# Kernel optimization log

Measured on AMD Instinct MI355X. Metric: run time of the kernel, lower is better.

The kernel has to match this reference:

```python
import jax, jax.numpy as jnp
import numpy as np
from jax import lax

D = 33            # n_vertices
NEG_SLOPE = 0.2   # LeakyReLU slope
EPS_IN = 1e-5     # InstanceNorm eps


def _block(x, w, b, gamma, beta):
    # Conv2d(k=3, stride=2, pad=1) -> LeakyReLU(0.2) -> optional InstanceNorm2d(affine)
    y = lax.conv_general_dilated(x, w, (2, 2), [(1, 1), (1, 1)],
                                 dimension_numbers=('NCHW', 'OIHW', 'NCHW'))
    y = y + b[None, :, None, None]
    y = jnp.where(y >= 0, y, NEG_SLOPE * y)
    if gamma is not None:
        mu = jnp.mean(y, (2, 3), keepdims=True)
        var = jnp.var(y, (2, 3), keepdims=True)
        y = (y - mu) * lax.rsqrt(var + EPS_IN) * gamma[None, :, None, None] + beta[None, :, None, None]
    return y


def _backbone(lq, w1, b1, g1, be1, w2, b2, g2, be2, w3, b3, g3, be3,
              w4, b4, g4, be4, w5, b5):
    B = lq.shape[0]
    # F.interpolate(..., 256, bilinear, align_corners=False) == half-pixel linear, no antialias
    x = jax.image.resize(lq, (B, 3, 256, 256), method='linear', antialias=False)
    x = _block(x, w1, b1, g1, be1)   # [B,16,128,128]
    x = _block(x, w2, b2, g2, be2)   # [B,32,64,64]
    x = _block(x, w3, b3, g3, be3)   # [B,64,32,32]
    x = _block(x, w4, b4, g4, be4)   # [B,128,16,16]
    x = _block(x, w5, b5, None, None)  # [B,128,8,8]; Dropout is identity in eval
    # AdaptiveAvgPool2d(2) on 8x8 -> mean over 4x4 blocks
    x = x.reshape(B, 128, 2, 4, 2, 4).mean((3, 5))  # [B,128,2,2]
    return x.reshape(B, -1)  # [B,512]


def _trilerp(lut, r, g, b):
    # lut [3,D,D,D]; r,g,b [N] in [0, D-1]; align_corners=True + border padding
    i0 = jnp.clip(jnp.floor(r).astype(jnp.int32), 0, D - 2)
    j0 = jnp.clip(jnp.floor(g).astype(jnp.int32), 0, D - 2)
    k0 = jnp.clip(jnp.floor(b).astype(jnp.int32), 0, D - 2)
    fr, fg, fb = r - i0, g - j0, b - k0

    def c(di, dj, dk):
        return lut[:, i0 + di, j0 + dj, k0 + dk]  # [3,N]

    return (c(0, 0, 0) * (1 - fr) * (1 - fg) * (1 - fb)
            + c(0, 0, 1) * (1 - fr) * (1 - fg) * fb
            + c(0, 1, 0) * (1 - fr) * fg * (1 - fb)
            + c(0, 1, 1) * (1 - fr) * fg * fb
            + c(1, 0, 0) * fr * (1 - fg) * (1 - fb)
            + c(1, 0, 1) * fr * (1 - fg) * fb
            + c(1, 1, 0) * fr * fg * (1 - fb)
            + c(1, 1, 1) * fr * fg * fb)


def _ailut_transform(img, luts, vertices):
    # img [B,3,H,W] in [0,1]; luts [B,3,D,D,D]; vertices [B,3,D] sorted in [0,1]
    B, C, H, W = img.shape
    p = img.reshape(B, C, -1)  # [B,3,N]
    # per-(b,c) searchsorted(right=True)
    idx = jax.vmap(jax.vmap(lambda v, x: jnp.searchsorted(v, x, side='right')))(vertices, p)
    idx = jnp.clip(idx, 1, D - 1)
    v_lo = jnp.take_along_axis(vertices, idx - 1, axis=-1)
    v_hi = jnp.take_along_axis(vertices, idx, axis=-1)
    frac = (p - v_lo) / (v_hi - v_lo + 1e-8)
    coord = (idx - 1).astype(img.dtype) + frac        # [B,3,N] in [0, D-1]
    coord = jnp.clip(coord, 0.0, D - 1.0)             # border padding
    # torch grid layout (blue->W, green->H, red->D); LUT axes are (red, green, blue)
    sampled = jax.vmap(_trilerp)(luts, coord[:, 0], coord[:, 1], coord[:, 2])  # [B,3,N]
    return sampled.reshape(B, C, H, W)


def _forward(lq, w1, b1, g1, be1, w2, b2, g2, be2, w3, b3, g3, be3,
             w4, b4, g4, be4, w5, b5, lw, lb, bw, aw, ab):
    B = lq.shape[0]
    codes = _backbone(lq, w1, b1, g1, be1, w2, b2, g2, be2, w3, b3, g3, be3,
                      w4, b4, g4, be4, w5, b5)          # [B,512]
    # LUTGenerator
    weights = codes @ lw.T + lb                          # [B,3]
    luts = (weights @ bw.T).reshape(B, 3, D, D, D)       # [B,3,D,D,D]
    # AdaInt
    intervals = (codes @ aw.T + ab).reshape(B, 3, D - 1)
    intervals = jax.nn.softmax(intervals, axis=-1)
    vertices = jnp.pad(jnp.cumsum(intervals, axis=-1), ((0, 0), (0, 0), (1, 0)))  # [B,3,D]
    outs = jnp.clip(_ailut_transform(lq, luts, vertices), 0.0, 1.0)
    return outs, weights, vertices


def setup_inputs() -> dict:
    key = jax.random.key(0)
    ks = jax.random.split(key, 16)
    B = 4
    lq = jax.random.uniform(ks[0], (B, 3, 1024, 1024), jnp.float32)

    def cw(k, o, i):
        return jax.random.normal(k, (o, i, 3, 3), jnp.float32) * (1.0 / np.sqrt(i * 9))

    w1 = cw(ks[1], 16, 3);   b1 = jnp.zeros(16);  g1 = jnp.ones(16);  be1 = jnp.zeros(16)
    w2 = cw(ks[2], 32, 16);  b2 = jnp.zeros(32);  g2 = jnp.ones(32);  be2 = jnp.zeros(32)
    w3 = cw(ks[3], 64, 32);  b3 = jnp.zeros(64);  g3 = jnp.ones(64);  be3 = jnp.zeros(64)
    w4 = cw(ks[4], 128, 64); b4 = jnp.zeros(128); g4 = jnp.ones(128); be4 = jnp.zeros(128)
    w5 = cw(ks[5], 128, 128); b5 = jnp.zeros(128)

    lw = jax.random.normal(ks[6], (3, 512), jnp.float32) * 0.02
    lb = jnp.ones(3, jnp.float32)  # init: bias = ones
    # basis LUT bank: rank0 = identity LUT (meshgrid/(D-1), channel-flipped), others small
    grid = jnp.stack(jnp.meshgrid(jnp.arange(D), jnp.arange(D), jnp.arange(D),
                                  indexing='ij'), 0).astype(jnp.float32) / (D - 1)
    identity = grid[::-1].reshape(-1, 1)  # [3*D^3,1]
    bw = jnp.concatenate([identity,
                          jax.random.normal(ks[7], (3 * D ** 3, 2), jnp.float32) * 0.01], axis=1)
    aw = jax.random.normal(ks[8], (96, 512), jnp.float32) * 0.01
    ab = jnp.ones(96, jnp.float32)  # init: bias = ones
    return {'lq': lq, 'w1': w1, 'b1': b1, 'g1': g1, 'be1': be1,
            'w2': w2, 'b2': b2, 'g2': g2, 'be2': be2,
            'w3': w3, 'b3': b3, 'g3': g3, 'be3': be3,
            'w4': w4, 'b4': b4, 'g4': g4, 'be4': be4,
            'w5': w5, 'b5': b5, 'lw': lw, 'lb': lb, 'bw': bw, 'aw': aw, 'ab': ab}


def reference(lq, w1, b1, g1, be1, w2, b2, g2, be2, w3, b3, g3, be3,
              w4, b4, g4, be4, w5, b5, lw, lb, bw, aw, ab):
    return _forward(lq, w1, b1, g1, be1, w2, b2, g2, be2, w3, b3, g3, be3,
                    w4, b4, g4, be4, w5, b5, lw, lb, bw, aw, ab)
```

## Files before the change

### kernel.cpp

```cpp
#include <hip/hip_runtime.h>
#include <math.h>

#define LUT_D 33
#define LUT_D3 35937
#define NEG 0.2f
#define BATCH 4
#define HW_IMG 1048576

__global__ void k_resize(const float* __restrict__ lq, float* __restrict__ out) {
    int gid = blockIdx.x * 256 + threadIdx.x;
    if (gid >= BATCH * 3 * 256 * 256) return;
    int x  = gid & 255;
    int y  = (gid >> 8) & 255;
    int pc = gid >> 16;
    const float* in = lq + (size_t)pc * HW_IMG;
    const float* p0 = in + (4 * y + 1) * 1024 + (4 * x + 1);
    out[gid] = 0.25f * (p0[0] + p0[1] + p0[1024] + p0[1025]);
}

template<int IC, int OC, int OH, int OW, int NSPLIT, bool NORM_IN, bool STATS_OUT>
__global__ void __launch_bounds__(256) k_conv_t(
    const float* __restrict__ in, const float* __restrict__ nrm_in,
    const float* __restrict__ w, const float* __restrict__ bias,
    float* __restrict__ out, float* __restrict__ part) {
    constexpr int IH = OH * 2, IW = OW * 2;
    constexpr int ICB = IC / NSPLIT;
    constexpr int TROW = 20, TSZ = 17 * TROW;
    constexpr int WQ = ICB * 9 / 4;
    constexpr int NTX = OW / 8, NTY = OH / 8, NOCG = OC / 16;
    constexpr int NT = NTX * NTY;
    constexpr int PX = OH * OW;

    __shared__ float sIn[ICB * TSZ];
    __shared__ float swl[16 * ICB * 9];
    __shared__ float sNm[NORM_IN ? ICB * 2 : 1];

    int id = blockIdx.x;
    int ocg   = id % NOCG;   id /= NOCG;
    int icc_i = id % NSPLIT; id /= NSPLIT;
    int tx    = id % NTX;    id /= NTX;
    int ty    = id % NTY;    id /= NTY;
    int b     = id;
    int icc   = icc_i * ICB;

    int t    = threadIdx.x;
    int lane = t >> 6;
    int px   = t & 63;
    int py   = px >> 3, pxx = px & 7;
    int oc0  = ocg * 16 + lane * 4;

    if (IC == ICB) {
        const float4* wsrc = (const float4*)(w + (size_t)ocg * 16 * IC * 9);
        for (int i = t; i < 16 * IC * 9 / 4; i += 256) ((float4*)swl)[i] = wsrc[i];
    } else {
        for (int i = t; i < 16 * WQ; i += 256) {
            int ol = i / WQ, qi = i % WQ;
            ((float4*)swl)[ol * WQ + qi] =
                *(const float4*)(w + ((size_t)(ocg * 16 + ol) * IC + icc) * 9 + qi * 4);
        }
    }
    if (NORM_IN) {
        for (int i = t; i < ICB * 2; i += 256) sNm[i] = nrm_in[(b * IC + icc) * 2 + i];
    }
    __syncthreads();

    int iy0 = ty * 16 - 1;
    int xbase = tx * 16;
    const float* inb = in + (size_t)(b * IC + icc) * (IH * IW);
    for (int q = t; q < ICB * 17 * 4; q += 256) {
        int ic_l = q / 68;
        int r    = q % 68;
        int row  = r >> 2, quad = r & 3;
        int iy = iy0 + row;
        float4 v = {0.f, 0.f, 0.f, 0.f};
        if (iy >= 0 && iy < IH) {
            v = *(const float4*)(inb + (size_t)ic_l * (IH * IW) + (size_t)iy * IW + xbase + quad * 4);
            if (NORM_IN) {
                float sc = sNm[ic_l * 2], sh = sNm[ic_l * 2 + 1];
                v.x = v.x * sc + sh; v.y = v.y * sc + sh;
                v.z = v.z * sc + sh; v.w = v.w * sc + sh;
            }
        }
        *(float4*)(sIn + ic_l * TSZ + row * TROW + 4 + quad * 4) = v;
    }
    for (int h = t; h < ICB * 17; h += 256) {
        int ic_l = h / 17, row = h % 17;
        int iy = iy0 + row, ix = xbase - 1;
        float v = 0.f;
        if (iy >= 0 && iy < IH && ix >= 0) {
            v = inb[(size_t)ic_l * (IH * IW) + (size_t)iy * IW + ix];
            if (NORM_IN) v = v * sNm[ic_l * 2] + sNm[ic_l * 2 + 1];
        }
        sIn[ic_l * TSZ + row * TROW + 3] = v;
    }
    __syncthreads();

    float acc[4];
    #pragma unroll
    for (int j = 0; j < 4; j++) acc[j] = (NSPLIT == 1) ? bias[oc0 + j] : 0.f;

    for (int i2 = 0; i2 < ICB; i2++) {
        const float* tp = sIn + i2 * TSZ + py * 2 * TROW + pxx * 2 + 3;
        float x0 = tp[0],        x1 = tp[1],        x2 = tp[2];
        float x3 = tp[TROW],     x4 = tp[TROW + 1], x5 = tp[TROW + 2];
        float x6 = tp[2 * TROW], x7 = tp[2 * TROW + 1], x8 = tp[2 * TROW + 2];
        #pragma unroll
        for (int j = 0; j < 4; j++) {
            const float* wp = swl + ((lane * 4 + j) * ICB + i2) * 9;
            acc[j] = fmaf(x0, wp[0], acc[j]);
            acc[j] = fmaf(x1, wp[1], acc[j]);
            acc[j] = fmaf(x2, wp[2], acc[j]);
            acc[j] = fmaf(x3, wp[3], acc[j]);
            acc[j] = fmaf(x4, wp[4], acc[j]);
            acc[j] = fmaf(x5, wp[5], acc[j]);
            acc[j] = fmaf(x6, wp[6], acc[j]);
            acc[j] = fmaf(x7, wp[7], acc[j]);
            acc[j] = fmaf(x8, wp[8], acc[j]);
        }
    }

    int oy = ty * 8 + py, ox = tx * 8 + pxx;
    if (NSPLIT == 1) {
        int tile = ty * NTX + tx;
        #pragma unroll
        for (int j = 0; j < 4; j++) {
            float a = acc[j];
            a = a >= 0.f ? a : NEG * a;
            out[((size_t)(b * OC + oc0 + j) * OH + oy) * OW + ox] = a;
            if (STATS_OUT) {
                float s1 = a, s2 = a * a;
                for (int off = 32; off > 0; off >>= 1) {
                    s1 += __shfl_down(s1, off, 64);
                    s2 += __shfl_down(s2, off, 64);
                }
                if (px == 0) {
                    size_t pi = ((size_t)(b * OC + oc0 + j) * NT + tile) * 2;
                    part[pi] = s1; part[pi + 1] = s2;
                }
            }
        }
    } else {
        #pragma unroll
        for (int j = 0; j < 4; j++) {
            part[(size_t)icc_i * (BATCH * OC * PX) +
                 (size_t)(b * OC + oc0 + j) * PX + oy * OW + ox] = acc[j];
        }
    }
}

template<int NSPLIT, int OC, int PX, bool STATS>
__global__ void k_combine(const float* __restrict__ ps, const float* __restrict__ bias,
                          float* __restrict__ out, float* __restrict__ spart) {
    constexpr int TOT = BATCH * OC * PX;
    int e = blockIdx.x * 256 + threadIdx.x;
    if (e >= TOT) return;
    float s = 0.f;
    #pragma unroll
    for (int k = 0; k < NSPLIT; k++) s += ps[(size_t)k * TOT + e];
    int oc = (e / PX) % OC;
    s += bias[oc];
    s = s >= 0.f ? s : NEG * s;
    out[e] = s;
    if (STATS) {
        float s1 = s, s2 = s * s;
        for (int off = 32; off > 0; off >>= 1) {
            s1 += __shfl_down(s1, off, 64);
            s2 += __shfl_down(s2, off, 64);
        }
        if ((threadIdx.x & 63) == 0) {
            int widx = e >> 6;
            spart[widx * 2] = s1; spart[widx * 2 + 1] = s2;
        }
    }
}

template<int NT>
__global__ void k_norm(const float* __restrict__ part, const float* __restrict__ g,
                       const float* __restrict__ be, float invN, int C,
                       float* __restrict__ nrm) {
    int bc = blockIdx.x;
    int t  = threadIdx.x;
    float s1 = 0.f, s2 = 0.f;
    for (int i = t; i < NT; i += 64) {
        s1 += part[((size_t)bc * NT + i) * 2];
        s2 += part[((size_t)bc * NT + i) * 2 + 1];
    }
    #pragma unroll
    for (int off = 32; off > 0; off >>= 1) {
        s1 += __shfl_down(s1, off, 64);
        s2 += __shfl_down(s2, off, 64);
    }
    if (t == 0) {
        int c = bc % C;
        float m   = s1 * invN;
        float var = s2 * invN - m * m;
        float sc  = g[c] * rsqrtf(var + 1e-5f);
        nrm[bc * 2]     = sc;
        nrm[bc * 2 + 1] = be[c] - m * sc;
    }
}

__global__ void k_pool(const float* __restrict__ f5, float* __restrict__ codes) {
    int c = blockIdx.x * 256 + threadIdx.x;
    if (c >= 2048) return;
    int b = c >> 9;
    int rest = c & 511;
    int oc = rest >> 2, q = rest & 3;
    int py = (q >> 1) * 4, px = (q & 1) * 4;
    const float* p = f5 + ((size_t)(b * 128 + oc)) * 64;
    float s = 0.f;
    #pragma unroll
    for (int dy = 0; dy < 4; dy++)
        #pragma unroll
        for (int dx = 0; dx < 4; dx++)
            s += p[(py + dy) * 8 + px + dx];
    codes[c] = s * (1.f / 16.f);
}

__global__ void k_head(const float* __restrict__ codes, const float* __restrict__ lw,
                       const float* __restrict__ lb, const float* __restrict__ aw,
                       const float* __restrict__ ab, float* __restrict__ wt,
                       float* __restrict__ vert, float* __restrict__ out_w,
                       float* __restrict__ out_v) {
    int blk = blockIdx.x;
    int t = threadIdx.x;
    if (blk == 12) {
        if (t < 12) {
            int b = t / 3, j = t % 3;
            const float* c = codes + b * 512;
            const float* l = lw + j * 512;
            float s = lb[j];
            for (int k = 0; k < 512; k++) s += c[k] * l[k];
            wt[t] = s;
            out_w[t] = s;
        }
        return;
    }
    int b = blk / 3, ch = blk % 3;
    __shared__ float y[32];
    if (t < 32) {
        const float* c = codes + b * 512;
        const float* a = aw + (size_t)(ch * 32 + t) * 512;
        float s = ab[ch * 32 + t];
        for (int k = 0; k < 512; k++) s += c[k] * a[k];
        y[t] = s;
    }
    __syncthreads();
    if (t == 0) {
        float mx = y[0];
        for (int m = 1; m < 32; m++) mx = fmaxf(mx, y[m]);
        float e[32];
        float sum = 0.f;
        for (int m = 0; m < 32; m++) { e[m] = expf(y[m] - mx); sum += e[m]; }
        float inv = 1.f / sum;
        float cum = 0.f;
        float* vb = vert + (b * 3 + ch) * 33;
        float* ob = out_v + (b * 3 + ch) * 33;
        vb[0] = 0.f; ob[0] = 0.f;
        for (int m = 0; m < 32; m++) { cum += e[m] * inv; vb[m + 1] = cum; ob[m + 1] = cum; }
    }
}

__global__ void k_lutgen(const float* __restrict__ bw, const float* __restrict__ wt,
                         float* __restrict__ luts4) {
    int gid = blockIdx.x * 256 + threadIdx.x;
    if (gid >= BATCH * LUT_D3) return;
    int b = gid / LUT_D3;
    int cell = gid - b * LUT_D3;
    float w0 = wt[b * 3], w1 = wt[b * 3 + 1], w2 = wt[b * 3 + 2];
    const float* r0 = bw + (size_t)(0 * LUT_D3 + cell) * 3;
    const float* r1 = bw + (size_t)(1 * LUT_D3 + cell) * 3;
    const float* r2 = bw + (size_t)(2 * LUT_D3 + cell) * 3;
    float4 o;
    o.x = r0[0] * w0 + r0[1] * w1 + r0[2] * w2;
    o.y = r1[0] * w0 + r1[1] * w1 + r1[2] * w2;
    o.z = r2[0] * w0 + r2[1] * w1 + r2[2] * w2;
    o.w = 0.f;
    ((float4*)luts4)[gid] = o;
}

__device__ __forceinline__ void search1(const float* __restrict__ sv, int ch, float x,
                                        int& i0, float& f) {
    const float* v = sv + ch * LUT_D;
    int lo = 0, hi = LUT_D;
    while (lo < hi) { int mid = (lo + hi) >> 1; if (v[mid] <= x) lo = mid + 1; else hi = mid; }
    int idx = lo < 1 ? 1 : (lo > LUT_D - 1 ? LUT_D - 1 : lo);
    float vl = v[idx - 1], vh = v[idx];
    float fr = (x - vl) / (vh - vl + 1e-8f);
    float coord = (float)(idx - 1) + fr;
    coord = fminf(fmaxf(coord, 0.f), (float)(LUT_D - 1));
    i0 = (int)floorf(coord);
    if (i0 > LUT_D - 2) i0 = LUT_D - 2;
    f = coord - (float)i0;
}

__global__ void __launch_bounds__(256) k_transform(const float* __restrict__ lq,
                                                   const float* __restrict__ luts4,
                                                   const float* __restrict__ vert,
                                                   float* __restrict__ out) {
    int bimg = blockIdx.x >> 10;
    int blk  = blockIdx.x & 1023;
    __shared__ float sv[3 * LUT_D];
    if (threadIdx.x < 3 * LUT_D) sv[threadIdx.x] = vert[bimg * 3 * LUT_D + threadIdx.x];
    __syncthreads();
    int p0 = blk * 1024 + threadIdx.x * 4;
    const float* lr = lq + (size_t)bimg * 3 * HW_IMG + p0;
    float4 r4 = *(const float4*)(lr);
    float4 g4 = *(const float4*)(lr + HW_IMG);
    float4 b4 = *(const float4*)(lr + 2 * HW_IMG);
    const float4* L = (const float4*)(luts4 + (size_t)bimg * LUT_D3 * 4);
    float rr[4] = {r4.x, r4.y, r4.z, r4.w};
    float gg[4] = {g4.x, g4.y, g4.z, g4.w};
    float bb[4] = {b4.x, b4.y, b4.z, b4.w};
    float ro[4], go[4], bo[4];
    #pragma unroll
    for (int i = 0; i < 4; i++) {
        int i0, j0, k0; float fr, fg, fb;
        search1(sv, 0, rr[i], i0, fr);
        search1(sv, 1, gg[i], j0, fg);
        search1(sv, 2, bb[i], k0, fb);
        int base = (i0 * LUT_D + j0) * LUT_D + k0;
        float4 q000 = L[base],        q001 = L[base + 1];
        float4 q010 = L[base + 33],   q011 = L[base + 34];
        float4 q100 = L[base + 1089], q101 = L[base + 1090];
        float4 q110 = L[base + 1122], q111 = L[base + 1123];
        float w000 = (1.f - fr) * (1.f - fg) * (1.f - fb), w001 = (1.f - fr) * (1.f - fg) * fb;
        float w010 = (1.f - fr) * fg * (1.f - fb),         w011 = (1.f - fr) * fg * fb;
        float w100 = fr * (1.f - fg) * (1.f - fb),         w101 = fr * (1.f - fg) * fb;
        float w110 = fr * fg * (1.f - fb),                 w111 = fr * fg * fb;
        float rx = q000.x*w000 + q001.x*w001 + q010.x*w010 + q011.x*w011
                 + q100.x*w100 + q101.x*w101 + q110.x*w110 + q111.x*w111;
        float ry = q000.y*w000 + q001.y*w001 + q010.y*w010 + q011.y*w011
                 + q100.y*w100 + q101.y*w101 + q110.y*w110 + q111.y*w111;
        float rz = q000.z*w000 + q001.z*w001 + q010.z*w010 + q011.z*w011
                 + q100.z*w100 + q101.z*w101 + q110.z*w110 + q111.z*w111;
        ro[i] = fminf(fmaxf(rx, 0.f), 1.f);
        go[i] = fminf(fmaxf(ry, 0.f), 1.f);
        bo[i] = fminf(fmaxf(rz, 0.f), 1.f);
    }
    float* op = out + (size_t)bimg * 3 * HW_IMG + p0;
    float4 o0 = {ro[0], ro[1], ro[2], ro[3]};
    float4 o1 = {go[0], go[1], go[2], go[3]};
    float4 o2 = {bo[0], bo[1], bo[2], bo[3]};
    *(float4*)(op) = o0;
    *(float4*)(op + HW_IMG) = o1;
    *(float4*)(op + 2 * HW_IMG) = o2;
}

extern "C" void kernel_launch(void* const* d_in, const int* in_sizes, int n_in,
                              void* d_out, int out_size, void* d_ws, size_t ws_size,
                              hipStream_t stream) {
    const float* lq  = (const float*)d_in[0];
    const float* w1  = (const float*)d_in[1];
    const float* b1  = (const float*)d_in[2];
    const float* g1  = (const float*)d_in[3];
    const float* be1 = (const float*)d_in[4];
    const float* w2  = (const float*)d_in[5];
    const float* b2  = (const float*)d_in[6];
    const float* g2  = (const float*)d_in[7];
    const float* be2 = (const float*)d_in[8];
    const float* w3  = (const float*)d_in[9];
    const float* b3  = (const float*)d_in[10];
    const float* g3  = (const float*)d_in[11];
    const float* be3 = (const float*)d_in[12];
    const float* w4  = (const float*)d_in[13];
    const float* b4  = (const float*)d_in[14];
    const float* g4  = (const float*)d_in[15];
    const float* be4 = (const float*)d_in[16];
    const float* w5  = (const float*)d_in[17];
    const float* b5  = (const float*)d_in[18];
    const float* lw  = (const float*)d_in[19];
    const float* lb  = (const float*)d_in[20];
    const float* bw  = (const float*)d_in[21];
    const float* aw  = (const float*)d_in[22];
    const float* ab  = (const float*)d_in[23];

    float* ws     = (float*)d_ws;
    float* r256   = ws;
    float* f1     = r256 + 786432;
    float* f2     = f1 + 1048576;
    float* f3     = f2 + 524288;
    float* f4     = f3 + 262144;
    float* f5     = f4 + 131072;
    float* codes  = f5 + 32768;
    float* wt     = codes + 2048;
    float* vert   = wt + 12;
    float* part1  = vert + 396;
    float* part2  = part1 + 32768;
    float* part3  = part2 + 16384;
    float* spart4 = part3 + 8192;
    float* norm1  = spart4 + 4096;
    float* norm2  = norm1 + 128;
    float* norm3  = norm2 + 256;
    float* norm4  = norm3 + 512;
    float* luts4  = norm4 + 1024;
    float* psplit4 = f1;
    float* psplit5 = f1 + 262144;

    float* outs  = (float*)d_out;
    float* out_w = outs + (size_t)BATCH * 3 * HW_IMG;
    float* out_v = out_w + 12;

    k_resize<<<3072, 256, 0, stream>>>(lq, r256);
    k_conv_t<3, 16, 128, 128, 1, false, true><<<1024, 256, 0, stream>>>(
        r256, nullptr, w1, b1, f1, part1);
    k_norm<256><<<64, 64, 0, stream>>>(part1, g1, be1, 1.f / 16384.f, 16, norm1);
    k_conv_t<16, 32, 64, 64, 1, true, true><<<512, 256, 0, stream>>>(
        f1, norm1, w2, b2, f2, part2);
    k_norm<64><<<128, 64, 0, stream>>>(part2, g2, be2, 1.f / 4096.f, 32, norm2);
    k_conv_t<32, 64, 32, 32, 1, true, true><<<256, 256, 0, stream>>>(
        f2, norm2, w3, b3, f3, part3);
    k_norm<16><<<256, 64, 0, stream>>>(part3, g3, be3, 1.f / 1024.f, 64, norm3);
    k_conv_t<64, 128, 16, 16, 2, true, false><<<256, 256, 0, stream>>>(
        f3, norm3, w4, b4, nullptr, psplit4);
    k_combine<2, 128, 256, true><<<512, 256, 0, stream>>>(psplit4, b4, f4, spart4);
    k_norm<4><<<512, 64, 0, stream>>>(spart4, g4, be4, 1.f / 256.f, 128, norm4);
    k_conv_t<128, 128, 8, 8, 4, true, false><<<128, 256, 0, stream>>>(
        f4, norm4, w5, b5, nullptr, psplit5);
    k_combine<4, 128, 64, false><<<128, 256, 0, stream>>>(psplit5, b5, f5, nullptr);
    k_pool<<<8, 256, 0, stream>>>(f5, codes);
    k_head<<<13, 64, 0, stream>>>(codes, lw, lb, aw, ab, wt, vert, out_w, out_v);
    k_lutgen<<<(BATCH * LUT_D3 + 255) / 256, 256, 0, stream>>>(bw, wt, luts4);
    k_transform<<<BATCH * 1024, 256, 0, stream>>>(lq, luts4, vert, outs);
}
```

Before: 320.5 us.

## Pack LUT as fp16 with k-neighbor pairs to halve trilinear gathers

```diff
diff --git a/kernel.cpp b/kernel.cpp
--- a/kernel.cpp
+++ b/kernel.cpp
@@ -1,4 +1,5 @@
 #include <hip/hip_runtime.h>
+#include <hip/hip_fp16.h>
 #include <math.h>
 
 #define LUT_D 33
@@ -262,21 +263,30 @@
 }
 
 __global__ void k_lutgen(const float* __restrict__ bw, const float* __restrict__ wt,
-                         float* __restrict__ luts4) {
+                         float4* __restrict__ lutp) {
     int gid = blockIdx.x * 256 + threadIdx.x;
     if (gid >= BATCH * LUT_D3) return;
     int b = gid / LUT_D3;
     int cell = gid - b * LUT_D3;
+    int k = cell % LUT_D;
+    int cn = (k < LUT_D - 1) ? cell + 1 : cell;
     float w0 = wt[b * 3], w1 = wt[b * 3 + 1], w2 = wt[b * 3 + 2];
-    const float* r0 = bw + (size_t)(0 * LUT_D3 + cell) * 3;
-    const float* r1 = bw + (size_t)(1 * LUT_D3 + cell) * 3;
-    const float* r2 = bw + (size_t)(2 * LUT_D3 + cell) * 3;
-    float4 o;
-    o.x = r0[0] * w0 + r0[1] * w1 + r0[2] * w2;
-    o.y = r1[0] * w0 + r1[1] * w1 + r1[2] * w2;
-    o.z = r2[0] * w0 + r2[1] * w1 + r2[2] * w2;
-    o.w = 0.f;
-    ((float4*)luts4)[gid] = o;
+    const float* r0p = bw + (size_t)(0 * LUT_D3 + cell) * 3;
+    const float* g0p = bw + (size_t)(1 * LUT_D3 + cell) * 3;
+    const float* b0p = bw + (size_t)(2 * LUT_D3 + cell) * 3;
+    const float* r1p = bw + (size_t)(0 * LUT_D3 + cn) * 3;
+    const float* g1p = bw + (size_t)(1 * LUT_D3 + cn) * 3;
+    const float* b1p = bw + (size_t)(2 * LUT_D3 + cn) * 3;
+    union { float4 f4; __half h[8]; } u;
+    u.h[0] = __float2half_rn(r0p[0] * w0 + r0p[1] * w1 + r0p[2] * w2);
+    u.h[1] = __float2half_rn(g0p[0] * w0 + g0p[1] * w1 + g0p[2] * w2);
+    u.h[2] = __float2half_rn(b0p[0] * w0 + b0p[1] * w1 + b0p[2] * w2);
+    u.h[3] = __float2half_rn(r1p[0] * w0 + r1p[1] * w1 + r1p[2] * w2);
+    u.h[4] = __float2half_rn(g1p[0] * w0 + g1p[1] * w1 + g1p[2] * w2);
+    u.h[5] = __float2half_rn(b1p[0] * w0 + b1p[1] * w1 + b1p[2] * w2);
+    u.h[6] = __float2half_rn(0.f);
+    u.h[7] = __float2half_rn(0.f);
+    lutp[gid] = u.f4;
 }
 
 __device__ __forceinline__ void search1(const float* __restrict__ sv, int ch, float x,
@@ -294,8 +304,20 @@
     f = coord - (float)i0;
 }
 
+__device__ __forceinline__ void decode_lerp(float4 e, float fb,
+                                            float& rv, float& gv, float& bv) {
+    union { float f; __half2 h; } u0, u1, u2;
+    u0.f = e.x; u1.f = e.y; u2.f = e.z;
+    float2 a = __half22float2(u0.h);
+    float2 b = __half22float2(u1.h);
+    float2 c = __half22float2(u2.h);
+    rv = fmaf(fb, b.y - a.x, a.x);
+    gv = fmaf(fb, c.x - a.y, a.y);
+    bv = fmaf(fb, c.y - b.x, b.x);
+}
+
 __global__ void __launch_bounds__(256) k_transform(const float* __restrict__ lq,
-                                                   const float* __restrict__ luts4,
+                                                   const float4* __restrict__ lutp,
                                                    const float* __restrict__ vert,
                                                    float* __restrict__ out) {
     int bimg = blockIdx.x >> 10;
@@ -308,7 +330,7 @@
     float4 r4 = *(const float4*)(lr);
     float4 g4 = *(const float4*)(lr + HW_IMG);
     float4 b4 = *(const float4*)(lr + 2 * HW_IMG);
-    const float4* L = (const float4*)(luts4 + (size_t)bimg * LUT_D3 * 4);
+    const float4* L = lutp + (size_t)bimg * LUT_D3;
     float rr[4] = {r4.x, r4.y, r4.z, r4.w};
     float gg[4] = {g4.x, g4.y, g4.z, g4.w};
     float bb[4] = {b4.x, b4.y, b4.z, b4.w};
@@ -320,20 +342,20 @@
         search1(sv, 1, gg[i], j0, fg);
         search1(sv, 2, bb[i], k0, fb);
         int base = (i0 * LUT_D + j0) * LUT_D + k0;
-        float4 q000 = L[base],        q001 = L[base + 1];
-        float4 q010 = L[base + 33],   q011 = L[base + 34];
-        float4 q100 = L[base + 1089], q101 = L[base + 1090];
-        float4 q110 = L[base + 1122], q111 = L[base + 1123];
-        float w000 = (1.f - fr) * (1.f - fg) * (1.f - fb), w001 = (1.f - fr) * (1.f - fg) * fb;
-        float w010 = (1.f - fr) * fg * (1.f - fb),         w011 = (1.f - fr) * fg * fb;
-        float w100 = fr * (1.f - fg) * (1.f - fb),         w101 = fr * (1.f - fg) * fb;
-        float w110 = fr * fg * (1.f - fb),                 w111 = fr * fg * fb;
-        float rx = q000.x*w000 + q001.x*w001 + q010.x*w010 + q011.x*w011
-                 + q100.x*w100 + q101.x*w101 + q110.x*w110 + q111.x*w111;
-        float ry = q000.y*w000 + q001.y*w001 + q010.y*w010 + q011.y*w011
-                 + q100.y*w100 + q101.y*w101 + q110.y*w110 + q111.y*w111;
-        float rz = q000.z*w000 + q001.z*w001 + q010.z*w010 + q011.z*w011
-                 + q100.z*w100 + q101.z*w101 + q110.z*w110 + q111.z*w111;
+        float4 e00 = L[base];
+        float4 e01 = L[base + 33];
+        float4 e10 = L[base + 1089];
+        float4 e11 = L[base + 1122];
+        float r00, g00, b00, r01, g01, b01, r10, g10, b10, r11, g11, b11;
+        decode_lerp(e00, fb, r00, g00, b00);
+        decode_lerp(e01, fb, r01, g01, b01);
+        decode_lerp(e10, fb, r10, g10, b10);
+        decode_lerp(e11, fb, r11, g11, b11);
+        float w00 = (1.f - fr) * (1.f - fg), w01 = (1.f - fr) * fg;
+        float w10 = fr * (1.f - fg),         w11 = fr * fg;
+        float rx = r00 * w00 + r01 * w01 + r10 * w10 + r11 * w11;
+        float ry = g00 * w00 + g01 * w01 + g10 * w10 + g11 * w11;
+        float rz = b00 * w00 + b01 * w01 + b10 * w10 + b11 * w11;
         ro[i] = fminf(fmaxf(rx, 0.f), 1.f);
         go[i] = fminf(fmaxf(ry, 0.f), 1.f);
         bo[i] = fminf(fmaxf(rz, 0.f), 1.f);
@@ -420,6 +442,6 @@
     k_combine<4, 128, 64, false><<<128, 256, 0, stream>>>(psplit5, b5, f5, nullptr);
     k_pool<<<8, 256, 0, stream>>>(f5, codes);
     k_head<<<13, 64, 0, stream>>>(codes, lw, lb, aw, ab, wt, vert, out_w, out_v);
-    k_lutgen<<<(BATCH * LUT_D3 + 255) / 256, 256, 0, stream>>>(bw, wt, luts4);
-    k_transform<<<BATCH * 1024, 256, 0, stream>>>(lq, luts4, vert, outs);
-}
+    k_lutgen<<<(BATCH * LUT_D3 + 255) / 256, 256, 0, stream>>>(bw, wt, (float4*)luts4);
+    k_transform<<<BATCH * 1024, 256, 0, stream>>>(lq, (const float4*)luts4, vert, outs);
+}
```

Measured after the change: 310.9 us. 3.0% less time.
